# Kernel optimization log

Hardware: AMD Instinct MI355X
Metric: run time of the kernel (lower is better)

Reference implementation:

```python
import jax, jax.numpy as jnp
import numpy as np
from jax import lax

THRESHOLD = 1.0  # threshold_potential from __init__
STRIDE = (1, 1)
PADDING = 'SAME'


def setup_inputs() -> dict:
    key = jax.random.key(0)
    k1, k2, k3 = jax.random.split(key, 3)
    input_to_layer = jax.random.normal(k1, (1, 512, 512, 16), dtype=jnp.float32)
    weights = jax.random.normal(k2, (3, 3, 16, 64), dtype=jnp.float32)
    old_potentials = jax.random.normal(k3, (1, 512, 512, 64), dtype=jnp.float32)
    return {
        'input_to_layer': input_to_layer,
        'weights': weights,
        'old_potentials': old_potentials,
    }


def reference(input_to_layer, weights, old_potentials):
    # conv2d NHWC x HWIO -> NHWC, SAME padding, stride 1 (as tf.nn.conv2d)
    out_conv = lax.conv_general_dilated(
        input_to_layer, weights,
        window_strides=STRIDE, padding=PADDING,
        dimension_numbers=('NHWC', 'HWIO', 'NHWC'))
    # accumulate membrane potential, fused threshold -> spike + reset
    new_potentials = out_conv + old_potentials
    spiked = new_potentials >= THRESHOLD
    curr_spikes = spiked.astype(new_potentials.dtype)
    new_potentials = jnp.where(spiked, 0.0, new_potentials)
    # original returns spikes; new_potentials is the updated state
    return curr_spikes, new_potentials
```

## Files before the change

kernel.cpp:

```cpp
#include <hip/hip_runtime.h>


#define H 512
#define W 512
#define CI 16
#define CO 64
#define TX 32
#define TY 8
#define LDS_XS 36

__global__ __launch_bounds__(256, 2)
void snn_conv_kernel(const float* __restrict__ in,
                     const float* __restrict__ w,
                     const float* __restrict__ oldp,
                     float* __restrict__ out_spk,
                     float* __restrict__ out_pot)
{
    __shared__ float s_in[(TY + 2) * CI * LDS_XS];
    __shared__ float s_w[9 * CI * CO];

    const int tid = threadIdx.x;
    const int bx = blockIdx.x & 15;
    const int by = blockIdx.x >> 4;
    const int tx0 = bx * TX;
    const int ty0 = by * TY;

    {
        const float4* wsrc = (const float4*)w;
        float4* wdst = (float4*)s_w;
        #pragma unroll
        for (int i = 0; i < 9; ++i)
            wdst[tid + i * 256] = wsrc[tid + i * 256];
    }

    for (int idx = tid; idx < (TY + 2) * (TX + 2); idx += 256) {
        const int ly = idx / (TX + 2);
        const int lx = idx - ly * (TX + 2);
        const int gy = ty0 + ly - 1;
        const int gx = tx0 + lx - 1;
        float4 v[4];
        if (gy >= 0 && gy < H && gx >= 0 && gx < W) {
            const float4* p = (const float4*)(in + (gy * W + gx) * CI);
            v[0] = p[0]; v[1] = p[1]; v[2] = p[2]; v[3] = p[3];
        } else {
            v[0] = v[1] = v[2] = v[3] = make_float4(0.f, 0.f, 0.f, 0.f);
        }
        const float* t = (const float*)v;
        float* dst = s_in + ly * (CI * LDS_XS) + lx;
        #pragma unroll
        for (int c = 0; c < CI; ++c)
            dst[c * LDS_XS] = t[c];
    }
    __syncthreads();

    const int cog = (tid & 7) * 8;
    const int pg  = tid >> 3;
    const int px  = (pg & 3) * 8;
    const int py  = pg >> 2;

    float acc[8][8];
    #pragma unroll
    for (int xi = 0; xi < 8; ++xi)
        #pragma unroll
        for (int c = 0; c < 8; ++c)
            acc[xi][c] = 0.f;

    for (int ky = 0; ky < 3; ++ky) {
        const float* irow = s_in + (py + ky) * (CI * LDS_XS) + px;
        const float* wrow = s_w + ky * 3 * CI * CO + cog;
        #pragma unroll 1
        for (int ci = 0; ci < CI; ++ci) {
            const float* ir = irow + ci * LDS_XS;
            float iv[10];
            *(float4*)&iv[0] = *(const float4*)(ir);
            *(float4*)&iv[4] = *(const float4*)(ir + 4);
            iv[8] = ir[8];
            iv[9] = ir[9];
            const float* wr = wrow + ci * CO;
            #pragma unroll
            for (int kx = 0; kx < 3; ++kx) {
                float wv[8];
                *(float4*)&wv[0] = *(const float4*)(wr + kx * CI * CO);
                *(float4*)&wv[4] = *(const float4*)(wr + kx * CI * CO + 4);
                #pragma unroll
                for (int xi = 0; xi < 8; ++xi)
                    #pragma unroll
                    for (int c = 0; c < 8; ++c)
                        acc[xi][c] = fmaf(iv[xi + kx], wv[c], acc[xi][c]);
            }
        }
    }

    const int gy = ty0 + py;
    #pragma unroll
    for (int xi = 0; xi < 8; ++xi) {
        const int gx = tx0 + px + xi;
        const int base = (gy * W + gx) * CO + cog;
        float old[8];
        *(float4*)&old[0] = *(const float4*)(oldp + base);
        *(float4*)&old[4] = *(const float4*)(oldp + base + 4);
        float spk[8], pot[8];
        #pragma unroll
        for (int c = 0; c < 8; ++c) {
            const float np = acc[xi][c] + old[c];
            const bool s = (np >= 1.0f);
            spk[c] = s ? 1.0f : 0.0f;
            pot[c] = s ? 0.0f : np;
        }
        *(float4*)(out_spk + base)     = *(const float4*)&spk[0];
        *(float4*)(out_spk + base + 4) = *(const float4*)&spk[4];
        *(float4*)(out_pot + base)     = *(const float4*)&pot[0];
        *(float4*)(out_pot + base + 4) = *(const float4*)&pot[4];
    }
}

extern "C" void kernel_launch(void* const* d_in, const int* in_sizes, int n_in,
                              void* d_out, int out_size, void* d_ws, size_t ws_size,
                              hipStream_t stream) {
    const float* in   = (const float*)d_in[0];
    const float* w    = (const float*)d_in[1];
    const float* oldp = (const float*)d_in[2];
    float* out_spk = (float*)d_out;
    float* out_pot = out_spk + (size_t)H * W * CO;

    const int grid = (W / TX) * (H / TY);
    snn_conv_kernel<<<grid, 256, 0, stream>>>(in, w, oldp, out_spk, out_pot);
}
```

Before: 227.3 us.

## Read weights from global memory, raise occupancy, use nontemporal loads/stores

Drops the 36KB shared-memory weight staging and reads weights straight from global memory (through L1/L2), which shrinks LDS per block and raises launch bounds to 4 blocks per CU. The inner ci loop is unrolled by 2, and the three kx weight vectors are loaded before the FMAs. The old-potential loads and output stores become nontemporal to avoid polluting the cache. The risk is that per-thread global weight loads add latency and cache traffic, and the higher occupancy target can force register spills with the 64-element accumulator.

```diff
diff --git a/kernel.cpp b/kernel.cpp
--- a/kernel.cpp
+++ b/kernel.cpp
@@ -9,7 +9,9 @@
 #define TY 8
 #define LDS_XS 36
 
-__global__ __launch_bounds__(256, 2)
+typedef float v4f __attribute__((ext_vector_type(4)));
+
+__global__ __launch_bounds__(256, 4)
 void snn_conv_kernel(const float* __restrict__ in,
                      const float* __restrict__ w,
                      const float* __restrict__ oldp,
@@ -17,7 +19,6 @@
                      float* __restrict__ out_pot)
 {
     __shared__ float s_in[(TY + 2) * CI * LDS_XS];
-    __shared__ float s_w[9 * CI * CO];
 
     const int tid = threadIdx.x;
     const int bx = blockIdx.x & 15;
@@ -25,25 +26,17 @@
     const int tx0 = bx * TX;
     const int ty0 = by * TY;
 
-    {
-        const float4* wsrc = (const float4*)w;
-        float4* wdst = (float4*)s_w;
-        #pragma unroll
-        for (int i = 0; i < 9; ++i)
-            wdst[tid + i * 256] = wsrc[tid + i * 256];
-    }
-
     for (int idx = tid; idx < (TY + 2) * (TX + 2); idx += 256) {
         const int ly = idx / (TX + 2);
         const int lx = idx - ly * (TX + 2);
         const int gy = ty0 + ly - 1;
         const int gx = tx0 + lx - 1;
-        float4 v[4];
+        v4f v[4];
         if (gy >= 0 && gy < H && gx >= 0 && gx < W) {
-            const float4* p = (const float4*)(in + (gy * W + gx) * CI);
+            const v4f* p = (const v4f*)(in + (gy * W + gx) * CI);
             v[0] = p[0]; v[1] = p[1]; v[2] = p[2]; v[3] = p[3];
         } else {
-            v[0] = v[1] = v[2] = v[3] = make_float4(0.f, 0.f, 0.f, 0.f);
+            v[0] = v[1] = v[2] = v[3] = (v4f)(0.f);
         }
         const float* t = (const float*)v;
         float* dst = s_in + ly * (CI * LDS_XS) + lx;
@@ -67,27 +60,29 @@
 
     for (int ky = 0; ky < 3; ++ky) {
         const float* irow = s_in + (py + ky) * (CI * LDS_XS) + px;
-        const float* wrow = s_w + ky * 3 * CI * CO + cog;
-        #pragma unroll 1
+        const float* wky = w + ky * 3 * CI * CO + cog;
+        #pragma unroll 2
         for (int ci = 0; ci < CI; ++ci) {
             const float* ir = irow + ci * LDS_XS;
             float iv[10];
-            *(float4*)&iv[0] = *(const float4*)(ir);
-            *(float4*)&iv[4] = *(const float4*)(ir + 4);
+            *(v4f*)&iv[0] = *(const v4f*)(ir);
+            *(v4f*)&iv[4] = *(const v4f*)(ir + 4);
             iv[8] = ir[8];
             iv[9] = ir[9];
-            const float* wr = wrow + ci * CO;
+            const float* wr = wky + ci * CO;
+            float wv[3][8];
             #pragma unroll
             for (int kx = 0; kx < 3; ++kx) {
-                float wv[8];
-                *(float4*)&wv[0] = *(const float4*)(wr + kx * CI * CO);
-                *(float4*)&wv[4] = *(const float4*)(wr + kx * CI * CO + 4);
+                *(v4f*)&wv[kx][0] = *(const v4f*)(wr + kx * CI * CO);
+                *(v4f*)&wv[kx][4] = *(const v4f*)(wr + kx * CI * CO + 4);
+            }
+            #pragma unroll
+            for (int kx = 0; kx < 3; ++kx)
                 #pragma unroll
                 for (int xi = 0; xi < 8; ++xi)
                     #pragma unroll
                     for (int c = 0; c < 8; ++c)
-                        acc[xi][c] = fmaf(iv[xi + kx], wv[c], acc[xi][c]);
-            }
+                        acc[xi][c] = fmaf(iv[xi + kx], wv[kx][c], acc[xi][c]);
         }
     }
 
@@ -96,9 +91,11 @@
     for (int xi = 0; xi < 8; ++xi) {
         const int gx = tx0 + px + xi;
         const int base = (gy * W + gx) * CO + cog;
+        v4f old0 = __builtin_nontemporal_load((const v4f*)(oldp + base));
+        v4f old1 = __builtin_nontemporal_load((const v4f*)(oldp + base) + 1);
         float old[8];
-        *(float4*)&old[0] = *(const float4*)(oldp + base);
-        *(float4*)&old[4] = *(const float4*)(oldp + base + 4);
+        *(v4f*)&old[0] = old0;
+        *(v4f*)&old[4] = old1;
         float spk[8], pot[8];
         #pragma unroll
         for (int c = 0; c < 8; ++c) {
@@ -107,10 +104,10 @@
             spk[c] = s ? 1.0f : 0.0f;
             pot[c] = s ? 0.0f : np;
         }
-        *(float4*)(out_spk + base)     = *(const float4*)&spk[0];
-        *(float4*)(out_spk + base + 4) = *(const float4*)&spk[4];
-        *(float4*)(out_pot + base)     = *(const float4*)&pot[0];
-        *(float4*)(out_pot + base + 4) = *(const float4*)&pot[4];
+        __builtin_nontemporal_store(*(const v4f*)&spk[0], (v4f*)(out_spk + base));
+        __builtin_nontemporal_store(*(const v4f*)&spk[4], (v4f*)(out_spk + base) + 1);
+        __builtin_nontemporal_store(*(const v4f*)&pot[0], (v4f*)(out_pot + base));
+        __builtin_nontemporal_store(*(const v4f*)&pot[4], (v4f*)(out_pot + base) + 1);
     }
 }
 
```

New measurement: 257.8 us. +13.4%, slower.
